# Kernel tuning notes

Measured on AMD Instinct MI355X. Metric: run time of the kernel, lower is better.

The kernel has to match this reference:

```python
import jax, jax.numpy as jnp
import numpy as np

ALPHA = 0.9
EPS = 0.01
LAMBDA_PENALTY = 1.0
THRESHOLD = 0.8
COS_EPS = 1e-8
N, F, E = 8192, 256, 262144


def setup_inputs() -> dict:
    key = jax.random.key(0)
    k1, k2, k3, k4, k5 = jax.random.split(key, 5)
    z = jax.random.normal(k1, (N, F), dtype=jnp.float32)
    x_hat = jax.random.normal(k2, (N, F), dtype=jnp.float32)
    edge_index = jax.random.randint(k3, (2, E), 0, N, dtype=jnp.int64)
    f_k2u = jax.random.randint(k4, (N,), 0, 6, dtype=jnp.int64)
    f_u2k = jax.random.randint(k5, (N,), 0, 32, dtype=jnp.int64)
    return {"z": z, "x_hat": x_hat, "edge_index": edge_index,
            "f_k2u": f_k2u, "f_u2k": f_u2k, "epoch": 10}


def _corrcoef_features(z):
    # torch.corrcoef(z.T): correlation between the F feature columns over N nodes
    zm = z - jnp.mean(z, axis=0, keepdims=True)        # [N, F]
    cov = zm.T @ zm                                    # [F, F] (scale cancels in corr)
    std = jnp.sqrt(jnp.diag(cov))                      # [F]
    cor = cov / (std[:, None] * std[None, :])
    cor = jnp.clip(jnp.nan_to_num(cor), -1.0, 1.0)
    # fill_diagonal_(0)
    return cor * (1.0 - jnp.eye(cor.shape[0], dtype=cor.dtype))


def reference(z, x_hat, edge_index, f_k2u, f_u2k, epoch):
    n, f = z.shape
    zm = z - jnp.mean(z, axis=0, keepdims=True)
    cor = _corrcoef_features(z)                        # [F, F]
    # per-node scalar weight: alpha**f_k2u + (1 - alpha**f_u2k)
    w = (ALPHA ** f_k2u.astype(z.dtype)
         + (1.0 - ALPHA ** f_u2k.astype(z.dtype)))     # [N]
    W = w[:, None] * zm                                # [N, F]
    z2 = z + EPS * (W @ cor)                           # [N, F]

    # homophily (crash=True): per-edge cosine sim, scatter-add by source, degree-normalize
    i, j = edge_index[0], edge_index[1]
    zi, zj = z2[i], z2[j]                              # [E, F] gathers
    num = jnp.sum(zi * zj, axis=1)
    ni = jnp.maximum(jnp.linalg.norm(zi, axis=1), COS_EPS)
    nj = jnp.maximum(jnp.linalg.norm(zj, axis=1), COS_EPS)
    sim = num / (ni * nj)                              # [E]
    scores = jax.ops.segment_sum(sim, i, num_segments=n)
    deg = jax.ops.segment_sum(jnp.ones_like(sim), i, num_segments=n)
    deg = jnp.where(deg == 0, 1.0, deg)
    homophily_loss = -jnp.mean(scores / deg)

    # extra_loss (crash=True): dense NxN similarity masked by dense adjacency
    sim_mat = z2 @ z2.T                                # [N, N]
    adj = jnp.zeros((n, n), dtype=z.dtype)
    adj = adj.at[i, j].set(1.0).at[j, i].set(1.0)
    non_conn = sim_mat * (1.0 - adj)
    penalty = jnp.mean(jnp.where(non_conn > THRESHOLD, non_conn, 0.0))

    return homophily_loss + LAMBDA_PENALTY * penalty
```

## Files before the change

### kernel.cpp

```cpp
#include <hip/hip_runtime.h>
#include <stdint.h>

#define EPS_C 0.01f
#define THRESH 0.8f

constexpr int Nn = 8192;
constexpr int Ff = 256;
constexpr int Ee = 262144;

__device__ __forceinline__ float b2f(unsigned short u) {
  union { uint32_t i; float f; } v; v.i = ((uint32_t)u) << 16; return v.f;
}
__device__ __forceinline__ unsigned short f2b(float f) {
  union { uint32_t i; float f; } v; v.f = f;
  uint32_t r = v.i + 0x7FFFu + ((v.i >> 16) & 1u);
  return (unsigned short)(r >> 16);
}

__global__ void k_colsum(const float* __restrict__ z, float* __restrict__ colsum) {
  int t = threadIdx.x;
  int r0 = blockIdx.x * 128;
  float acc = 0.f;
#pragma unroll 8
  for (int r = 0; r < 128; ++r)
    acc += z[(size_t)(r0 + r) * Ff + t];
  atomicAdd(&colsum[t], acc);
}

__global__ void k_w(const int* __restrict__ k2u, const int* __restrict__ u2k,
                    float* __restrict__ w) {
  int n = blockIdx.x * 256 + threadIdx.x;
  w[n] = powf(0.9f, (float)k2u[n]) + 1.f - powf(0.9f, (float)u2k[n]);
}

__global__ void k_transpose(const float* __restrict__ z, unsigned short* __restrict__ zT) {
  __shared__ float Ls[64][65];
  int n0 = blockIdx.x * 64;
  int c0 = blockIdx.y * 64;
  int t = threadIdx.x;
  int r = t >> 4;
  int cq = t & 15;
#pragma unroll
  for (int i = 0; i < 4; ++i) {
    int row = r + 16 * i;
    float4 v = *(const float4*)(z + (size_t)(n0 + row) * Ff + c0 + cq * 4);
    Ls[row][cq * 4 + 0] = v.x;
    Ls[row][cq * 4 + 1] = v.y;
    Ls[row][cq * 4 + 2] = v.z;
    Ls[row][cq * 4 + 3] = v.w;
  }
  __syncthreads();
  int cr = t >> 4;
  int nq = t & 15;
#pragma unroll
  for (int i = 0; i < 4; ++i) {
    int c = cr + 16 * i;
    ushort4 o;
    o.x = f2b(Ls[nq * 4 + 0][c]);
    o.y = f2b(Ls[nq * 4 + 1][c]);
    o.z = f2b(Ls[nq * 4 + 2][c]);
    o.w = f2b(Ls[nq * 4 + 3][c]);
    *(ushort4*)(zT + (size_t)(c0 + c) * Nn + n0 + nq * 4) = o;
  }
}

typedef __bf16 bf16x8 __attribute__((ext_vector_type(8)));
typedef float f32x4 __attribute__((ext_vector_type(4)));

__global__ __launch_bounds__(256, 2) void k_covg(const unsigned short* __restrict__ zT,
                                                 float* __restrict__ covp) {
  int bx = blockIdx.x, by = blockIdx.y, p = blockIdx.z;
  __shared__ __align__(16) unsigned short As[128 * 64];
  __shared__ __align__(16) unsigned short Bs[128 * 64];
  int t = threadIdx.x;
  int lane = t & 63, wv = t >> 6;
  int wr = wv >> 1, wc = wv & 1;
  int quad = lane >> 4, l15 = lane & 15;
  int a0 = by * 128, b0 = bx * 128;

  f32x4 acc[4][4];
#pragma unroll
  for (int i = 0; i < 4; ++i)
#pragma unroll
    for (int j = 0; j < 4; ++j) acc[i][j] = (f32x4){0.f, 0.f, 0.f, 0.f};

  for (int kk = 0; kk < 8; ++kk) {
    int k0 = p * 512 + kk * 64;
#pragma unroll
    for (int it = 0; it < 4; ++it) {
      int s = it * 256 + t;
      int r = s >> 3;
      int g = (s & 7) ^ (r & 7);
      const unsigned short* ga = zT + (size_t)(a0 + r) * Nn + k0 + g * 8;
      const unsigned short* gb = zT + (size_t)(b0 + r) * Nn + k0 + g * 8;
      __builtin_amdgcn_global_load_lds((const __attribute__((address_space(1))) void*)ga,
                                       (__attribute__((address_space(3))) void*)(As + s * 8),
                                       16, 0, 0);
      __builtin_amdgcn_global_load_lds((const __attribute__((address_space(1))) void*)gb,
                                       (__attribute__((address_space(3))) void*)(Bs + s * 8),
                                       16, 0, 0);
    }
    __syncthreads();
#pragma unroll
    for (int kc = 0; kc < 2; ++kc) {
      bf16x8 afr[4], bfr[4];
#pragma unroll
      for (int mt = 0; mt < 4; ++mt) {
        int rA = wr * 64 + mt * 16 + l15;
        int g = kc * 4 + quad;
        int gl = g ^ (rA & 7);
        afr[mt] = *(const bf16x8*)(As + ((size_t)rA * 8 + gl) * 8);
      }
#pragma unroll
      for (int nt = 0; nt < 4; ++nt) {
        int rB = wc * 64 + nt * 16 + l15;
        int g = kc * 4 + quad;
        int gl = g ^ (rB & 7);
        bfr[nt] = *(const bf16x8*)(Bs + ((size_t)rB * 8 + gl) * 8);
      }
#pragma unroll
      for (int mt = 0; mt < 4; ++mt)
#pragma unroll
        for (int nt = 0; nt < 4; ++nt)
          acc[mt][nt] = __builtin_amdgcn_mfma_f32_16x16x32_bf16(afr[mt], bfr[nt],
                                                                acc[mt][nt], 0, 0, 0);
    }
    __syncthreads();
  }

  float* outp = covp + (size_t)p * 65536;
#pragma unroll
  for (int mt = 0; mt < 4; ++mt)
#pragma unroll
    for (int r = 0; r < 4; ++r) {
      int a = a0 + wr * 64 + mt * 16 + quad * 4 + r;
#pragma unroll
      for (int nt = 0; nt < 4; ++nt) {
        int b = b0 + wc * 64 + nt * 16 + l15;
        outp[(size_t)a * Ff + b] = acc[mt][nt][r];
      }
    }
}

__global__ void k_diag(const float* __restrict__ covp, const float* __restrict__ colsum,
                       float* __restrict__ stdv) {
  int a = threadIdx.x;
  float m = colsum[a] * (1.f / 8192.f);
  float s = -8192.f * m * m;
#pragma unroll
  for (int p = 0; p < 16; ++p) s += covp[(size_t)p * 65536 + a * Ff + a];
  stdv[a] = sqrtf(s);
}

__global__ void k_cor(const float* __restrict__ covp, const float* __restrict__ colsum,
                      const float* __restrict__ stdv, float* __restrict__ cor) {
  int idx = blockIdx.x * 256 + threadIdx.x;
  int a = idx >> 8, b = idx & 255;
  float c = 0.f;
  if (a != b) {
    float g = 0.f;
#pragma unroll
    for (int p = 0; p < 16; ++p) g += covp[(size_t)p * 65536 + idx];
    float cv = g - 8192.f * (colsum[a] * (1.f / 8192.f)) * (colsum[b] * (1.f / 8192.f));
    c = cv / (stdv[a] * stdv[b]);
    if (c != c) c = 0.f;
    c = fminf(1.f, fmaxf(-1.f, c));
  }
  cor[idx] = c;
}

__global__ __launch_bounds__(256) void k_z2(const float* __restrict__ z,
    const float* __restrict__ colsum, const float* __restrict__ w,
    const float* __restrict__ cor, unsigned short* __restrict__ z2b,
    float* __restrict__ norms) {
  __shared__ float Wl[32 * 256];
  int t = threadIdx.x;
  int row0 = blockIdx.x * 32;
  float mt = colsum[t] * (1.f / 8192.f);
  for (int rr = 0; rr < 32; ++rr) {
    int row = row0 + rr;
    Wl[rr * 256 + t] = w[row] * (z[(size_t)row * Ff + t] - mt);
  }
  __syncthreads();
  int tc = t & 63, tr = t >> 6;
  float acc[8][4];
#pragma unroll
  for (int i = 0; i < 8; ++i)
#pragma unroll
    for (int j = 0; j < 4; ++j) acc[i][j] = 0.f;
  const float* corc = cor + tc * 4;
  for (int k = 0; k < 256; ++k) {
    float4 c4 = *(const float4*)(corc + (size_t)k * 256);
#pragma unroll
    for (int rr = 0; rr < 8; ++rr) {
      float wv = Wl[(tr * 8 + rr) * 256 + k];
      acc[rr][0] = fmaf(wv, c4.x, acc[rr][0]);
      acc[rr][1] = fmaf(wv, c4.y, acc[rr][1]);
      acc[rr][2] = fmaf(wv, c4.z, acc[rr][2]);
      acc[rr][3] = fmaf(wv, c4.w, acc[rr][3]);
    }
  }
#pragma unroll
  for (int rr = 0; rr < 8; ++rr) {
    int row = row0 + tr * 8 + rr;
    float4 zv = *(const float4*)(z + (size_t)row * Ff + tc * 4);
    float x0 = zv.x + EPS_C * acc[rr][0];
    float x1 = zv.y + EPS_C * acc[rr][1];
    float x2 = zv.z + EPS_C * acc[rr][2];
    float x3 = zv.w + EPS_C * acc[rr][3];
    ushort4 o;
    o.x = f2b(x0); o.y = f2b(x1); o.z = f2b(x2); o.w = f2b(x3);
    *(ushort4*)(z2b + (size_t)row * Ff + tc * 4) = o;
    float s = x0 * x0 + x1 * x1 + x2 * x2 + x3 * x3;
#pragma unroll
    for (int m = 1; m < 64; m <<= 1) s += __shfl_xor(s, m);
    if (tc == 0) norms[row] = fmaxf(sqrtf(s), 1e-8f);
  }
}

__global__ void k_adj(const int* __restrict__ ei, const int* __restrict__ ej,
                      unsigned int* __restrict__ adj) {
  int e = blockIdx.x * 256 + threadIdx.x;
  unsigned int i = (unsigned int)ei[e], j = (unsigned int)ej[e];
  size_t b1 = (size_t)i * Nn + j;
  size_t b2 = (size_t)j * Nn + i;
  atomicOr(&adj[b1 >> 5], 1u << (b1 & 31));
  atomicOr(&adj[b2 >> 5], 1u << (b2 & 31));
}

__global__ __launch_bounds__(256) void k_edge(const int* __restrict__ ei,
                       const int* __restrict__ ej,
                       const unsigned short* __restrict__ z2b,
                       const float* __restrict__ norms,
                       float* __restrict__ scores, float* __restrict__ deg) {
  int t = threadIdx.x;
  int wv = t >> 6, lane = t & 63;
  int half = lane >> 5;
  int l32 = lane & 31;
  int gw = blockIdx.x * 4 + wv;
  int ebase = gw * 32;
#pragma unroll 2
  for (int it = 0; it < 16; ++it) {
    int e = ebase + it * 2 + half;
    int i = ei[e], j = ej[e];
    uint4 ua = *(const uint4*)(z2b + (size_t)i * Ff + l32 * 8);
    uint4 ub = *(const uint4*)(z2b + (size_t)j * Ff + l32 * 8);
    float d = 0.f;
    const uint32_t* pa = (const uint32_t*)&ua;
    const uint32_t* pb = (const uint32_t*)&ub;
#pragma unroll
    for (int q = 0; q < 4; ++q) {
      union { uint32_t u; float f; } alo, ahi, blo, bhi;
      alo.u = pa[q] << 16;  ahi.u = pa[q] & 0xffff0000u;
      blo.u = pb[q] << 16;  bhi.u = pb[q] & 0xffff0000u;
      d = fmaf(alo.f, blo.f, d);
      d = fmaf(ahi.f, bhi.f, d);
    }
#pragma unroll
    for (int m = 1; m < 32; m <<= 1) d += __shfl_xor(d, m);
    if (l32 == 0) {
      float sim = d / (norms[i] * norms[j]);
      atomicAdd(&scores[i], sim);
      atomicAdd(&deg[i], 1.f);
    }
  }
}

__global__ void k_homo(const float* __restrict__ scores, const float* __restrict__ deg,
                       double* __restrict__ hsum) {
  __shared__ float red[4];
  int n = blockIdx.x * 256 + threadIdx.x;
  float dg = deg[n];
  float v = scores[n] / (dg == 0.f ? 1.f : dg);
#pragma unroll
  for (int m = 1; m < 64; m <<= 1) v += __shfl_xor(v, m);
  int lane = threadIdx.x & 63, wv = threadIdx.x >> 6;
  if (lane == 0) red[wv] = v;
  __syncthreads();
  if (threadIdx.x == 0) atomicAdd(hsum, (double)(red[0] + red[1] + red[2] + red[3]));
}

__global__ __launch_bounds__(256, 2) void k_penalty(const unsigned short* __restrict__ z2b,
    const unsigned int* __restrict__ adj, double* __restrict__ psum) {
  int bc = blockIdx.x, br = blockIdx.y;
  if (br > bc) return;
  __shared__ __align__(16) unsigned short As[128 * 64];
  __shared__ __align__(16) unsigned short Bs[128 * 64];
  __shared__ float red[4];
  int t = threadIdx.x;
  int lane = t & 63;
  int wv = t >> 6;
  int wr = wv >> 1, wc = wv & 1;
  int quad = lane >> 4;
  int l15 = lane & 15;
  int arow0 = br * 128, brow0 = bc * 128;

  f32x4 acc[4][4];
#pragma unroll
  for (int i = 0; i < 4; ++i)
#pragma unroll
    for (int j = 0; j < 4; ++j) acc[i][j] = (f32x4){0.f, 0.f, 0.f, 0.f};

  for (int kk = 0; kk < 4; ++kk) {
    int k0 = kk * 64;
#pragma unroll
    for (int it = 0; it < 4; ++it) {
      int s = it * 256 + t;
      int r = s >> 3;
      int g = (s & 7) ^ (r & 7);
      const unsigned short* ga = z2b + (size_t)(arow0 + r) * Ff + k0 + g * 8;
      const unsigned short* gb = z2b + (size_t)(brow0 + r) * Ff + k0 + g * 8;
      __builtin_amdgcn_global_load_lds((const __attribute__((address_space(1))) void*)ga,
                                       (__attribute__((address_space(3))) void*)(As + s * 8),
                                       16, 0, 0);
      __builtin_amdgcn_global_load_lds((const __attribute__((address_space(1))) void*)gb,
                                       (__attribute__((address_space(3))) void*)(Bs + s * 8),
                                       16, 0, 0);
    }
    __syncthreads();
#pragma unroll
    for (int kc = 0; kc < 2; ++kc) {
      bf16x8 afr[4], bfr[4];
#pragma unroll
      for (int mt = 0; mt < 4; ++mt) {
        int rA = wr * 64 + mt * 16 + l15;
        int g = kc * 4 + quad;
        int gl = g ^ (rA & 7);
        afr[mt] = *(const bf16x8*)(As + ((size_t)rA * 8 + gl) * 8);
      }
#pragma unroll
      for (int nt = 0; nt < 4; ++nt) {
        int rB = wc * 64 + nt * 16 + l15;
        int g = kc * 4 + quad;
        int gl = g ^ (rB & 7);
        bfr[nt] = *(const bf16x8*)(Bs + ((size_t)rB * 8 + gl) * 8);
      }
#pragma unroll
      for (int mt = 0; mt < 4; ++mt)
#pragma unroll
        for (int nt = 0; nt < 4; ++nt)
          acc[mt][nt] = __builtin_amdgcn_mfma_f32_16x16x32_bf16(afr[mt], bfr[nt],
                                                                acc[mt][nt], 0, 0, 0);
    }
    __syncthreads();
  }

  float local = 0.f;
  int a_base = arow0 + wr * 64;
  int b_base = brow0 + wc * 64;
#pragma unroll
  for (int mt = 0; mt < 4; ++mt) {
#pragma unroll
    for (int r = 0; r < 4; ++r) {
      int a = a_base + mt * 16 + quad * 4 + r;
      uint64_t bits = *(const uint64_t*)(adj + (size_t)a * 256 + (b_base >> 5));
#pragma unroll
      for (int nt = 0; nt < 4; ++nt) {
        float v = acc[mt][nt][r];
        int boff = nt * 16 + l15;
        bool conn = (bits >> boff) & 1ull;
        float wgt;
        if (br != bc) wgt = 2.f;
        else {
          int b = b_base + boff;
          wgt = (a < b) ? 2.f : (a == b ? 1.f : 0.f);
        }
        if (!conn && v > THRESH) local += wgt * v;
      }
    }
  }
#pragma unroll
  for (int m = 1; m < 64; m <<= 1) local += __shfl_xor(local, m);
  if (lane == 0) red[wv] = local;
  __syncthreads();
  if (t == 0) atomicAdd(psum, (double)(red[0] + red[1] + red[2] + red[3]));
}

__global__ void k_final(const double* __restrict__ hsum, const double* __restrict__ psum,
                        float* __restrict__ out) {
  if (threadIdx.x == 0) {
    double h = -(*hsum) / 8192.0;
    double p = (*psum) / (8192.0 * 8192.0);
    out[0] = (float)(h + p);
  }
}

extern "C" void kernel_launch(void* const* d_in, const int* in_sizes, int n_in,
                              void* d_out, int out_size, void* d_ws, size_t ws_size,
                              hipStream_t stream) {
  const float* z = (const float*)d_in[0];
  const int* ei = (const int*)d_in[2];
  const int* ej = ei + Ee;
  const int* k2u = (const int*)d_in[3];
  const int* u2k = (const int*)d_in[4];

  char* ws = (char*)d_ws;
  unsigned int* adj = (unsigned int*)(ws);
  float* colsum     = (float*)(ws + 8388608);
  float* scores     = (float*)(ws + 8389632);
  float* deg        = (float*)(ws + 8422400);
  double* psum      = (double*)(ws + 8455168);
  double* hsum      = (double*)(ws + 8455176);
  const size_t ZERO_BYTES = 8455184;
  float* covp       = (float*)(ws + 8455296);
  unsigned short* zT  = (unsigned short*)(ws + 12649600);
  unsigned short* z2b = (unsigned short*)(ws + 16843904);
  float* cor        = (float*)(ws + 21038208);
  float* w          = (float*)(ws + 21300352);
  float* norms      = (float*)(ws + 21333120);
  float* stdv       = (float*)(ws + 21365888);

  hipMemsetAsync(d_ws, 0, ZERO_BYTES, stream);
  k_colsum<<<64, 256, 0, stream>>>(z, colsum);
  k_w<<<32, 256, 0, stream>>>(k2u, u2k, w);
  k_adj<<<1024, 256, 0, stream>>>(ei, ej, adj);
  k_transpose<<<dim3(128, 4), 256, 0, stream>>>(z, zT);
  k_covg<<<dim3(2, 2, 16), 256, 0, stream>>>(zT, covp);
  k_diag<<<1, 256, 0, stream>>>(covp, colsum, stdv);
  k_cor<<<256, 256, 0, stream>>>(covp, colsum, stdv, cor);
  k_z2<<<256, 256, 0, stream>>>(z, colsum, w, cor, z2b, norms);
  k_edge<<<2048, 256, 0, stream>>>(ei, ej, z2b, norms, scores, deg);
  k_homo<<<32, 256, 0, stream>>>(scores, deg, hsum);
  k_penalty<<<dim3(64, 64), 256, 0, stream>>>(z2b, adj, psum);
  k_final<<<1, 64, 0, stream>>>(hsum, psum, (float*)d_out);
}
```

Measured before the change: 232.6 us.

## Fuse small kernels, double-buffer penalty GEMM loads, launch only upper-triangle tiles

Folds the column-sum into the transpose, the weight computation into k_z2, the std computation into k_cor, and the homophily reduction into k_final, removing four launches. The penalty kernel now launches only the 2080 upper-triangle tiles via a closed-form index mapping instead of 4096 blocks with early exit. Its K-loop is double-buffered, with explicit waitcnt and barriers so global-to-LDS loads overlap MFMA work. The cost is doubled LDS per block, which may reduce occupancy, plus redundant diagonal reads in every k_cor block.

```diff
diff --git a/kernel.cpp b/kernel.cpp
--- a/kernel.cpp
+++ b/kernel.cpp
@@ -1,5 +1,6 @@
 #include <hip/hip_runtime.h>
 #include <stdint.h>
+#include <math.h>
 
 #define EPS_C 0.01f
 #define THRESH 0.8f
@@ -17,23 +18,11 @@
   return (unsigned short)(r >> 16);
 }
 
-__global__ void k_colsum(const float* __restrict__ z, float* __restrict__ colsum) {
-  int t = threadIdx.x;
-  int r0 = blockIdx.x * 128;
-  float acc = 0.f;
-#pragma unroll 8
-  for (int r = 0; r < 128; ++r)
-    acc += z[(size_t)(r0 + r) * Ff + t];
-  atomicAdd(&colsum[t], acc);
-}
-
-__global__ void k_w(const int* __restrict__ k2u, const int* __restrict__ u2k,
-                    float* __restrict__ w) {
-  int n = blockIdx.x * 256 + threadIdx.x;
-  w[n] = powf(0.9f, (float)k2u[n]) + 1.f - powf(0.9f, (float)u2k[n]);
-}
-
-__global__ void k_transpose(const float* __restrict__ z, unsigned short* __restrict__ zT) {
+typedef __bf16 bf16x8 __attribute__((ext_vector_type(8)));
+typedef float f32x4 __attribute__((ext_vector_type(4)));
+
+__global__ void k_transpose(const float* __restrict__ z, unsigned short* __restrict__ zT,
+                            float* __restrict__ colsum) {
   __shared__ float Ls[64][65];
   int n0 = blockIdx.x * 64;
   int c0 = blockIdx.y * 64;
@@ -50,6 +39,12 @@
     Ls[row][cq * 4 + 3] = v.w;
   }
   __syncthreads();
+  if (t < 64) {
+    float s = 0.f;
+#pragma unroll
+    for (int rr = 0; rr < 64; ++rr) s += Ls[rr][t];
+    atomicAdd(&colsum[c0 + t], s);
+  }
   int cr = t >> 4;
   int nq = t & 15;
 #pragma unroll
@@ -63,9 +58,6 @@
     *(ushort4*)(zT + (size_t)(c0 + c) * Nn + n0 + nq * 4) = o;
   }
 }
-
-typedef __bf16 bf16x8 __attribute__((ext_vector_type(8)));
-typedef float f32x4 __attribute__((ext_vector_type(4)));
 
 __global__ __launch_bounds__(256, 2) void k_covg(const unsigned short* __restrict__ zT,
                                                  float* __restrict__ covp) {
@@ -142,44 +134,48 @@
     }
 }
 
-__global__ void k_diag(const float* __restrict__ covp, const float* __restrict__ colsum,
-                       float* __restrict__ stdv) {
-  int a = threadIdx.x;
-  float m = colsum[a] * (1.f / 8192.f);
-  float s = -8192.f * m * m;
-#pragma unroll
-  for (int p = 0; p < 16; ++p) s += covp[(size_t)p * 65536 + a * Ff + a];
-  stdv[a] = sqrtf(s);
-}
-
 __global__ void k_cor(const float* __restrict__ covp, const float* __restrict__ colsum,
-                      const float* __restrict__ stdv, float* __restrict__ cor) {
-  int idx = blockIdx.x * 256 + threadIdx.x;
-  int a = idx >> 8, b = idx & 255;
+                      float* __restrict__ cor) {
+  __shared__ float sd[256];
+  int a = blockIdx.x, b = threadIdx.x;
+  float mb = colsum[b] * (1.f / 8192.f);
+  float gb = 0.f;
+#pragma unroll
+  for (int p = 0; p < 16; ++p) gb += covp[(size_t)p * 65536 + b * 257];
+  float sb = sqrtf(gb - 8192.f * mb * mb);
+  sd[b] = sb;
+  float g = 0.f;
+#pragma unroll
+  for (int p = 0; p < 16; ++p) g += covp[(size_t)p * 65536 + a * Ff + b];
+  __syncthreads();
   float c = 0.f;
   if (a != b) {
-    float g = 0.f;
-#pragma unroll
-    for (int p = 0; p < 16; ++p) g += covp[(size_t)p * 65536 + idx];
-    float cv = g - 8192.f * (colsum[a] * (1.f / 8192.f)) * (colsum[b] * (1.f / 8192.f));
-    c = cv / (stdv[a] * stdv[b]);
+    float ma = colsum[a] * (1.f / 8192.f);
+    float cv = g - 8192.f * ma * mb;
+    c = cv / (sd[a] * sb);
     if (c != c) c = 0.f;
     c = fminf(1.f, fmaxf(-1.f, c));
   }
-  cor[idx] = c;
+  cor[a * Ff + b] = c;
 }
 
 __global__ __launch_bounds__(256) void k_z2(const float* __restrict__ z,
-    const float* __restrict__ colsum, const float* __restrict__ w,
-    const float* __restrict__ cor, unsigned short* __restrict__ z2b,
-    float* __restrict__ norms) {
+    const float* __restrict__ colsum, const int* __restrict__ k2u,
+    const int* __restrict__ u2k, const float* __restrict__ cor,
+    unsigned short* __restrict__ z2b, float* __restrict__ norms) {
   __shared__ float Wl[32 * 256];
+  __shared__ float ws_[32];
   int t = threadIdx.x;
   int row0 = blockIdx.x * 32;
+  if (t < 32) {
+    int row = row0 + t;
+    ws_[t] = powf(0.9f, (float)k2u[row]) + 1.f - powf(0.9f, (float)u2k[row]);
+  }
+  __syncthreads();
   float mt = colsum[t] * (1.f / 8192.f);
   for (int rr = 0; rr < 32; ++rr) {
     int row = row0 + rr;
-    Wl[rr * 256 + t] = w[row] * (z[(size_t)row * Ff + t] - mt);
+    Wl[rr * 256 + t] = ws_[rr] * (z[(size_t)row * Ff + t] - mt);
   }
   __syncthreads();
   int tc = t & 63, tr = t >> 6;
@@ -266,27 +262,15 @@
   }
 }
 
-__global__ void k_homo(const float* __restrict__ scores, const float* __restrict__ deg,
-                       double* __restrict__ hsum) {
-  __shared__ float red[4];
-  int n = blockIdx.x * 256 + threadIdx.x;
-  float dg = deg[n];
-  float v = scores[n] / (dg == 0.f ? 1.f : dg);
-#pragma unroll
-  for (int m = 1; m < 64; m <<= 1) v += __shfl_xor(v, m);
-  int lane = threadIdx.x & 63, wv = threadIdx.x >> 6;
-  if (lane == 0) red[wv] = v;
-  __syncthreads();
-  if (threadIdx.x == 0) atomicAdd(hsum, (double)(red[0] + red[1] + red[2] + red[3]));
-}
-
 __global__ __launch_bounds__(256, 2) void k_penalty(const unsigned short* __restrict__ z2b,
     const unsigned int* __restrict__ adj, double* __restrict__ psum) {
-  int bc = blockIdx.x, br = blockIdx.y;
-  if (br > bc) return;
-  __shared__ __align__(16) unsigned short As[128 * 64];
-  __shared__ __align__(16) unsigned short Bs[128 * 64];
-  __shared__ float red[4];
+  int tb = blockIdx.x;
+  int br = (int)(64.5 - sqrt(64.5 * 64.5 - 2.0 * (double)tb));
+  while ((br + 1) * 64 - ((br + 1) * br) / 2 <= tb) ++br;
+  while (br * 64 - (br * (br - 1)) / 2 > tb) --br;
+  int bc = br + (tb - (br * 64 - (br * (br - 1)) / 2));
+
+  __shared__ __align__(16) unsigned short LB[32768];
   int t = threadIdx.x;
   int lane = t & 63;
   int wv = t >> 6;
@@ -301,23 +285,35 @@
 #pragma unroll
     for (int j = 0; j < 4; ++j) acc[i][j] = (f32x4){0.f, 0.f, 0.f, 0.f};
 
-  for (int kk = 0; kk < 4; ++kk) {
-    int k0 = kk * 64;
-#pragma unroll
-    for (int it = 0; it < 4; ++it) {
-      int s = it * 256 + t;
-      int r = s >> 3;
-      int g = (s & 7) ^ (r & 7);
-      const unsigned short* ga = z2b + (size_t)(arow0 + r) * Ff + k0 + g * 8;
-      const unsigned short* gb = z2b + (size_t)(brow0 + r) * Ff + k0 + g * 8;
-      __builtin_amdgcn_global_load_lds((const __attribute__((address_space(1))) void*)ga,
-                                       (__attribute__((address_space(3))) void*)(As + s * 8),
-                                       16, 0, 0);
-      __builtin_amdgcn_global_load_lds((const __attribute__((address_space(1))) void*)gb,
-                                       (__attribute__((address_space(3))) void*)(Bs + s * 8),
-                                       16, 0, 0);
-    }
-    __syncthreads();
+#define ISSUE_PHASE(p)                                                                   \
+  {                                                                                      \
+    unsigned short* buf = LB + ((p) & 1) * 16384;                                        \
+    int k0 = (p) * 64;                                                                   \
+    _Pragma("unroll")                                                                    \
+    for (int it = 0; it < 4; ++it) {                                                     \
+      int s = it * 256 + t;                                                              \
+      int r = s >> 3;                                                                    \
+      int g = (s & 7) ^ (r & 7);                                                         \
+      const unsigned short* ga = z2b + (size_t)(arow0 + r) * Ff + k0 + g * 8;            \
+      const unsigned short* gb = z2b + (size_t)(brow0 + r) * Ff + k0 + g * 8;            \
+      __builtin_amdgcn_global_load_lds((const __attribute__((address_space(1))) void*)ga,\
+                                       (__attribute__((address_space(3))) void*)(buf + s * 8),      \
+                                       16, 0, 0);                                        \
+      __builtin_amdgcn_global_load_lds((const __attribute__((address_space(1))) void*)gb,\
+                                       (__attribute__((address_space(3))) void*)(buf + 8192 + s * 8),\
+                                       16, 0, 0);                                        \
+    }                                                                                    \
+  }
+
+  ISSUE_PHASE(0)
+  ISSUE_PHASE(1)
+#pragma unroll
+  for (int p = 0; p < 4; ++p) {
+    if (p < 3) __builtin_amdgcn_s_waitcnt(0xF78);
+    else       __builtin_amdgcn_s_waitcnt(0xF70);
+    __builtin_amdgcn_s_barrier();
+    const unsigned short* As = LB + (p & 1) * 16384;
+    const unsigned short* Bs = As + 8192;
 #pragma unroll
     for (int kc = 0; kc < 2; ++kc) {
       bf16x8 afr[4], bfr[4];
@@ -342,8 +338,10 @@
           acc[mt][nt] = __builtin_amdgcn_mfma_f32_16x16x32_bf16(afr[mt], bfr[nt],
                                                                 acc[mt][nt], 0, 0, 0);
     }
-    __syncthreads();
-  }
+    __builtin_amdgcn_s_barrier();
+    if (p < 2) ISSUE_PHASE(p + 2)
+  }
+#undef ISSUE_PHASE
 
   float local = 0.f;
   int a_base = arow0 + wr * 64;
@@ -371,15 +369,30 @@
   }
 #pragma unroll
   for (int m = 1; m < 64; m <<= 1) local += __shfl_xor(local, m);
+  __syncthreads();
+  float* red = (float*)LB;
   if (lane == 0) red[wv] = local;
   __syncthreads();
   if (t == 0) atomicAdd(psum, (double)(red[0] + red[1] + red[2] + red[3]));
 }
 
-__global__ void k_final(const double* __restrict__ hsum, const double* __restrict__ psum,
-                        float* __restrict__ out) {
-  if (threadIdx.x == 0) {
-    double h = -(*hsum) / 8192.0;
+__global__ void k_final(const float* __restrict__ scores, const float* __restrict__ deg,
+                        const double* __restrict__ psum, float* __restrict__ out) {
+  __shared__ float red[4];
+  int t = threadIdx.x;
+  float acc = 0.f;
+#pragma unroll 4
+  for (int it = 0; it < 32; ++it) {
+    int n = it * 256 + t;
+    float dg = deg[n];
+    acc += scores[n] / (dg == 0.f ? 1.f : dg);
+  }
+#pragma unroll
+  for (int m = 1; m < 64; m <<= 1) acc += __shfl_xor(acc, m);
+  if ((t & 63) == 0) red[t >> 6] = acc;
+  __syncthreads();
+  if (t == 0) {
+    double h = -(double)(red[0] + red[1] + red[2] + red[3]) / 8192.0;
     double p = (*psum) / (8192.0 * 8192.0);
     out[0] = (float)(h + p);
   }
@@ -400,27 +413,20 @@
   float* scores     = (float*)(ws + 8389632);
   float* deg        = (float*)(ws + 8422400);
   double* psum      = (double*)(ws + 8455168);
-  double* hsum      = (double*)(ws + 8455176);
-  const size_t ZERO_BYTES = 8455184;
+  const size_t ZERO_BYTES = 8455176;
   float* covp       = (float*)(ws + 8455296);
   unsigned short* zT  = (unsigned short*)(ws + 12649600);
   unsigned short* z2b = (unsigned short*)(ws + 16843904);
   float* cor        = (float*)(ws + 21038208);
-  float* w          = (float*)(ws + 21300352);
-  float* norms      = (float*)(ws + 21333120);
-  float* stdv       = (float*)(ws + 21365888);
+  float* norms      = (float*)(ws + 21300352);
 
   hipMemsetAsync(d_ws, 0, ZERO_BYTES, stream);
-  k_colsum<<<64, 256, 0, stream>>>(z, colsum);
-  k_w<<<32, 256, 0, stream>>>(k2u, u2k, w);
   k_adj<<<1024, 256, 0, stream>>>(ei, ej, adj);
-  k_transpose<<<dim3(128, 4), 256, 0, stream>>>(z, zT);
+  k_transpose<<<dim3(128, 4), 256, 0, stream>>>(z, zT, colsum);
   k_covg<<<dim3(2, 2, 16), 256, 0, stream>>>(zT, covp);
-  k_diag<<<1, 256, 0, stream>>>(covp, colsum, stdv);
-  k_cor<<<256, 256, 0, stream>>>(covp, colsum, stdv, cor);
-  k_z2<<<256, 256, 0, stream>>>(z, colsum, w, cor, z2b, norms);
+  k_cor<<<256, 256, 0, stream>>>(covp, colsum, cor);
+  k_z2<<<256, 256, 0, stream>>>(z, colsum, k2u, u2k, cor, z2b, norms);
   k_edge<<<2048, 256, 0, stream>>>(ei, ej, z2b, norms, scores, deg);
-  k_homo<<<32, 256, 0, stream>>>(scores, deg, hsum);
-  k_penalty<<<dim3(64, 64), 256, 0, stream>>>(z2b, adj, psum);
-  k_final<<<1, 64, 0, stream>>>(hsum, psum, (float*)d_out);
-}
+  k_penalty<<<2080, 256, 0, stream>>>(z2b, adj, psum);
+  k_final<<<1, 256, 0, stream>>>(scores, deg, psum, (float*)d_out);
+}
```

Result: faster. 224.6 us (-3.4%).
